# Performance work log

Measured on AMD Instinct MI355X. Metric: run time of the kernel, lower is better.

Reference implementation:

```python
import jax, jax.numpy as jnp
import numpy as np

N_NODES = 50000
N_EDGES = 800000
C = 96
L = 3


def setup_inputs() -> dict:
    key = jax.random.key(0)
    ks = jax.random.split(key, 7)
    x = jax.random.normal(ks[0], (N_NODES, C), dtype=jnp.float32)
    edge_index = jax.random.randint(ks[1], (2, N_EDGES), 0, N_NODES, dtype=jnp.int32)
    weight = jax.random.normal(ks[2], (L, C, C), dtype=jnp.float32) * (1.0 / np.sqrt(C))
    w_ih = jax.random.normal(ks[3], (3 * C, C), dtype=jnp.float32) * (1.0 / np.sqrt(C))
    w_hh = jax.random.normal(ks[4], (3 * C, C), dtype=jnp.float32) * (1.0 / np.sqrt(C))
    b_ih = jax.random.normal(ks[5], (3 * C,), dtype=jnp.float32) * 0.01
    b_hh = jax.random.normal(ks[6], (3 * C,), dtype=jnp.float32) * 0.01
    return {"x": x, "edge_index": edge_index, "weight": weight,
            "w_ih": w_ih, "w_hh": w_hh, "b_ih": b_ih, "b_hh": b_hh}


def _gru_cell(m, h, w_ih, w_hh, b_ih, b_hh):
    # PyTorch GRUCell math. gi/gh: [N, 3C]
    gi = m @ w_ih.T + b_ih
    gh = h @ w_hh.T + b_hh
    i_r, i_z, i_n = jnp.split(gi, 3, axis=-1)
    h_r, h_z, h_n = jnp.split(gh, 3, axis=-1)
    r = jax.nn.sigmoid(i_r + h_r)
    z = jax.nn.sigmoid(i_z + h_z)
    n = jnp.tanh(i_n + r * h_n)
    return (1.0 - z) * n + z * h


def reference(x, edge_index, weight, w_ih, w_hh, b_ih, b_hh):
    src = edge_index[0]  # message source (x_j)
    dst = edge_index[1]  # aggregation target
    for i in range(L):
        m = x @ weight[i]                                        # [N, C]
        agg = jax.ops.segment_sum(m[src], dst, num_segments=N_NODES)  # scatter-add
        x = _gru_cell(agg, x, w_ih, w_hh, b_ih, b_hh)
    return x
```

## Files before the change

kernel.cpp:

```cpp
#include <hip/hip_runtime.h>
#include <hip/hip_bf16.h>
#include <stdint.h>

#define NN 50000
#define NE 800000
#define CC 96
#define NL 3
#define NMT 3125

#define CAP 64
#define CAPSH 6

#define ELEMS_PER_LAYER 55296

#define FILL_GROUPS 8
#define FILL_GROUP_BLOCKS 400
#define FILL_BLOCKS (FILL_GROUPS*FILL_GROUP_BLOCKS)
#define NODES_PER_GROUP (NN/FILL_GROUPS)

#define PREP_ITEMS (NN*CC/8 + NL*288*CC + 288*CC)
#define PREP_BLOCKS ((PREP_ITEMS + 255)/256)

typedef _Float16 f16x8 __attribute__((ext_vector_type(8)));
typedef float f32x4 __attribute__((ext_vector_type(4)));
typedef uint16_t u16x8 __attribute__((ext_vector_type(8)));

__device__ __forceinline__ uint16_t f2h(float f){
  _Float16 h = (_Float16)f;
  return __builtin_bit_cast(uint16_t, h);
}
__device__ __forceinline__ float h2f(uint16_t u){
  return (float)__builtin_bit_cast(_Float16, u);
}

__device__ __forceinline__ size_t frag_elem(int tcol, int g2, int ks, int lane, int j){
  return (((size_t)(tcol*6 + g2)*3 + ks)*64 + lane)*8 + j;
}

__global__ void k_setup(const int* __restrict__ srcv, const int* __restrict__ dstv,
                        int* __restrict__ cursor, uint16_t* __restrict__ ssrc,
                        const float4* __restrict__ x, u16x8* __restrict__ xh,
                        const float* __restrict__ weight, const float* __restrict__ w_ih,
                        const float* __restrict__ w_hh, uint16_t* __restrict__ gw){
  if(blockIdx.x < FILL_BLOCKS){
    int g  = blockIdx.x & 7;
    int bg = blockIdx.x >> 3;
    int dlo = g * NODES_PER_GROUP;
    int dhi = dlo + NODES_PER_GROUP;
    const int tpg = FILL_GROUP_BLOCKS*256;
    for(int e = bg*256 + threadIdx.x; e < NE; e += tpg){
      int d = dstv[e];
      if(d >= dlo && d < dhi){
        int s = srcv[e];
        int pos = atomicAdd(&cursor[d], 1);
        if(pos < CAP) ssrc[((size_t)d << CAPSH) + pos] = (uint16_t)s;
      }
    }
    return;
  }
  int idx = (blockIdx.x - FILL_BLOCKS)*256 + threadIdx.x;
  const int N8 = NN*CC/8;
  if(idx < N8){
    float4 a = x[idx*2], b = x[idx*2+1];
    u16x8 o;
    o[0]=f2h(a.x); o[1]=f2h(a.y); o[2]=f2h(a.z); o[3]=f2h(a.w);
    o[4]=f2h(b.x); o[5]=f2h(b.y); o[6]=f2h(b.z); o[7]=f2h(b.w);
    xh[idx] = o;
    return;
  }
  int pidx = idx - N8;
  const int TOT1 = NL*288*CC;
  const int TOT2 = 288*CC;
  if(pidx < TOT1){
    int k = pidx % CC;
    int col = (pidx / CC) % 288;
    int l = pidx / (CC*288);
    const float4* wr = (const float4*)(weight + (size_t)(l*CC + k)*CC);
    const float4* ir = (const float4*)(w_ih + (size_t)col*CC);
    float acc = 0.f;
    #pragma unroll 4
    for(int k2=0;k2<CC/4;k2++){
      float4 a = wr[k2], b = ir[k2];
      acc += a.x*b.x + a.y*b.y + a.z*b.z + a.w*b.w;
    }
    int g = col / 96, cg = col % 96;
    int tcol = cg >> 4, n = cg & 15;
    int ks = k >> 5, r = (k & 31) >> 3, j = k & 7;
    int lane = r*16 + n;
    gw[(size_t)l*ELEMS_PER_LAYER + frag_elem(tcol, g, ks, lane, j)] = f2h(acc);
  } else {
    int idx2 = pidx - TOT1;
    if(idx2 < TOT2){
      int k = idx2 % CC;
      int col = idx2 / CC;
      uint16_t h = f2h(w_hh[(size_t)col*CC + k]);
      int g = col / 96, cg = col % 96;
      int tcol = cg >> 4, n = cg & 15;
      int ks = k >> 5, r = (k & 31) >> 3, j = k & 7;
      int lane = r*16 + n;
      size_t fe = frag_elem(tcol, 3+g, ks, lane, j);
      #pragma unroll
      for(int l=0;l<NL;l++) gw[(size_t)l*ELEMS_PER_LAYER + fe] = h;
    }
  }
}

#define MFMA16(A,B,C) __builtin_amdgcn_mfma_f32_16x16x32_f16(A,B,C,0,0,0)

__global__ __launch_bounds__(1024) void k_layer(
    const uint16_t* __restrict__ xh_cur, uint16_t* __restrict__ xh_nxt,
    const int* __restrict__ counts, const uint16_t* __restrict__ ssrc,
    const uint16_t* __restrict__ gw_l,
    const float* __restrict__ b_ih, const float* __restrict__ b_hh,
    float* __restrict__ out_f)
{
  __shared__ __align__(16) uint16_t lw[ELEMS_PER_LAYER];
  __shared__ u16x8 aggl[12*256];

  const int tid = threadIdx.x;
  const int wave = tid >> 6;
  const int lane = tid & 63;
  const int nidx = lane & 15;
  const int quad = lane >> 4;
  const int mtile = wave*256 + blockIdx.x;
  const bool valid = (mtile < NMT);
  const int mt = valid ? mtile : 0;

  f16x8 ax[3];
  {
    size_t arow = (size_t)(mt*16 + nidx)*CC;
    #pragma unroll
    for(int ks=0; ks<3; ks++)
      ax[ks] = *reinterpret_cast<const f16x8*>(xh_cur + arow + ks*32 + quad*8);
  }

  {
    const uint4* src = (const uint4*)gw_l;
    uint4* dst = (uint4*)lw;
    #pragma unroll
    for(int i=0;i<7;i++){
      int chunk = i*1024 + tid;
      if(chunk < ELEMS_PER_LAYER/8) dst[chunk] = src[chunk];
    }
  }

  {
    int nl_ = tid >> 2;
    int c8b = (tid & 3)*3;
    if(valid){
      int node = mt*16 + (nl_ & 15);
      int cnt = counts[node]; if(cnt > CAP) cnt = CAP;
      const u16x8* xg = (const u16x8*)xh_cur;
      float a0[8], a1[8], a2[8];
      #pragma unroll
      for(int t=0;t<8;t++){ a0[t]=0.f; a1[t]=0.f; a2[t]=0.f; }
      int j0 = node << CAPSH;
      int j1 = j0 + cnt;
      int j = j0;
      for(; j+4 <= j1; j+=4){
        ushort4 sv = *reinterpret_cast<const ushort4*>(ssrc + j);
        size_t b0 = (size_t)sv.x*12 + c8b;
        size_t b1 = (size_t)sv.y*12 + c8b;
        size_t b2 = (size_t)sv.z*12 + c8b;
        size_t b3 = (size_t)sv.w*12 + c8b;
        u16x8 v00=xg[b0], v01=xg[b0+1], v02=xg[b0+2];
        u16x8 v10=xg[b1], v11=xg[b1+1], v12=xg[b1+2];
        u16x8 v20=xg[b2], v21=xg[b2+1], v22=xg[b2+2];
        u16x8 v30=xg[b3], v31=xg[b3+1], v32=xg[b3+2];
        #pragma unroll
        for(int t=0;t<8;t++){
          a0[t] += (h2f(v00[t])+h2f(v10[t])) + (h2f(v20[t])+h2f(v30[t]));
          a1[t] += (h2f(v01[t])+h2f(v11[t])) + (h2f(v21[t])+h2f(v31[t]));
          a2[t] += (h2f(v02[t])+h2f(v12[t])) + (h2f(v22[t])+h2f(v32[t]));
        }
      }
      for(; j < j1; j++){
        size_t b = (size_t)ssrc[j]*12 + c8b;
        u16x8 v0=xg[b], v1=xg[b+1], v2=xg[b+2];
        #pragma unroll
        for(int t=0;t<8;t++){ a0[t]+=h2f(v0[t]); a1[t]+=h2f(v1[t]); a2[t]+=h2f(v2[t]); }
      }
      u16x8 w0, w1, w2;
      #pragma unroll
      for(int t=0;t<8;t++){ w0[t]=f2h(a0[t]); w1[t]=f2h(a1[t]); w2[t]=f2h(a2[t]); }
      aggl[(c8b+0)*256 + nl_] = w0;
      aggl[(c8b+1)*256 + nl_] = w1;
      aggl[(c8b+2)*256 + nl_] = w2;
    }
  }
  __syncthreads();
  if(!valid) return;

  f16x8 as[3];
  #pragma unroll
  for(int ks=0; ks<3; ks++)
    as[ks] = *reinterpret_cast<const f16x8*>(&aggl[(ks*4+quad)*256 + wave*16 + nidx]);

  #pragma unroll 1
  for(int tcol=0; tcol<6; tcol++){
    f32x4 air = {0.f,0.f,0.f,0.f}, aiz = {0.f,0.f,0.f,0.f}, ain = {0.f,0.f,0.f,0.f};
    f32x4 ahr = {0.f,0.f,0.f,0.f}, ahz = {0.f,0.f,0.f,0.f}, ahn = {0.f,0.f,0.f,0.f};

    #pragma unroll
    for(int ks=0; ks<3; ks++){
      const uint16_t* base = lw + (((size_t)tcol*6)*3 + ks)*512 + lane*8;
      #define BFRAG(g2) (*reinterpret_cast<const f16x8*>(base + (size_t)(g2)*3*512))
      air = MFMA16(as[ks], BFRAG(0), air);
      aiz = MFMA16(as[ks], BFRAG(1), aiz);
      ain = MFMA16(as[ks], BFRAG(2), ain);
      ahr = MFMA16(ax[ks], BFRAG(3), ahr);
      ahz = MFMA16(ax[ks], BFRAG(4), ahz);
      ahn = MFMA16(ax[ks], BFRAG(5), ahn);
      #undef BFRAG
    }

    int c = tcol*16 + nidx;
    float bir_ = b_ih[c], biz_ = b_ih[CC+c], bin_ = b_ih[2*CC+c];
    float bhr_ = b_hh[c], bhz_ = b_hh[CC+c], bhn_ = b_hh[2*CC+c];

    #pragma unroll
    for(int r=0;r<4;r++){
      int node = mtile*16 + quad*4 + r;
      float ir  = air[r] + bir_;
      float iz  = aiz[r] + biz_;
      float in_ = ain[r] + bin_;
      float hr  = ahr[r] + bhr_;
      float hz  = ahz[r] + bhz_;
      float hn  = ahn[r] + bhn_;
      float rg = 1.f/(1.f + __expf(-(ir+hr)));
      float zg = 1.f/(1.f + __expf(-(iz+hz)));
      float nv = in_ + rg*hn;
      float av = fminf(fabsf(nv), 15.f);
      float e2 = __expf(2.f*av);
      float tg = 1.f - 2.f/(e2 + 1.f);
      tg = (nv < 0.f)? -tg : tg;
      size_t oi = (size_t)node*CC + c;
      float hp = h2f(xh_cur[oi]);
      float h = (1.f - zg)*tg + zg*hp;
      if(out_f) out_f[oi] = h;
      else      xh_nxt[oi] = f2h(h);
    }
  }
}

extern "C" void kernel_launch(void* const* d_in, const int* in_sizes, int n_in,
                              void* d_out, int out_size, void* d_ws, size_t ws_size,
                              hipStream_t stream){
  const float* x0     = (const float*)d_in[0];
  const int*   ei     = (const int*)d_in[1];
  const float* weight = (const float*)d_in[2];
  const float* w_ih   = (const float*)d_in[3];
  const float* w_hh   = (const float*)d_in[4];
  const float* b_ih   = (const float*)d_in[5];
  const float* b_hh   = (const float*)d_in[6];
  float* out = (float*)d_out;

  const int* srcv = ei;
  const int* dstv = ei + NE;

  char* ws = (char*)d_ws;
  size_t off = 0;
  auto carve = [&](size_t bytes)->char*{
    char* p = ws + off;
    off += (bytes + 255) & ~(size_t)255;
    return p;
  };
  int* cursor     = (int*)carve((size_t)NN*4);
  uint16_t* ssrc  = (uint16_t*)carve((size_t)NN*CAP*2);
  uint16_t* xh16A = (uint16_t*)carve((size_t)NN*CC*2);
  uint16_t* xh16B = (uint16_t*)carve((size_t)NN*CC*2);
  uint16_t* gw    = (uint16_t*)carve((size_t)NL*ELEMS_PER_LAYER*2);

  hipMemsetAsync(cursor, 0, (size_t)NN*4, stream);
  k_setup<<<FILL_BLOCKS + PREP_BLOCKS, 256, 0, stream>>>(
      srcv, dstv, cursor, ssrc, (const float4*)x0, (u16x8*)xh16A, weight, w_ih, w_hh, gw);

  uint16_t* xh_cur = xh16A;
  uint16_t* xh_nxt = xh16B;
  for(int l=0; l<NL; l++){
    float* out_f = (l==NL-1) ? out : nullptr;
    k_layer<<<256, 1024, 0, stream>>>(xh_cur, xh_nxt, cursor, ssrc,
                                      gw + (size_t)l*ELEMS_PER_LAYER,
                                      b_ih, b_hh, out_f);
    uint16_t* t = xh_cur; xh_cur = xh_nxt; xh_nxt = t;
  }
}
```

Baseline: 256.6 us.

## Fuse setup and all layers into one cooperative persistent kernel with grid syncs

Replaces the separate setup kernel and the three per-layer launches with a single cooperative kernel of 256x1024 threads that uses grid.sync between phases. The CSR fill and the fp16 conversion/weight prep now run as grid-stride loops inside it. The aggregation is remapped so each lane gathers directly into its MFMA A-fragment layout, which removes the LDS staging buffer for the aggregate. The intent is to cut launch gaps and the LDS round trip. The cost is grid-wide barriers, reliance on cooperative launch residency, and far fewer threads doing the atomic edge-fill phase.

```diff
diff --git a/kernel.cpp b/kernel.cpp
--- a/kernel.cpp
+++ b/kernel.cpp
@@ -1,6 +1,8 @@
 #include <hip/hip_runtime.h>
-#include <hip/hip_bf16.h>
+#include <hip/hip_cooperative_groups.h>
 #include <stdint.h>
+
+namespace cg = cooperative_groups;
 
 #define NN 50000
 #define NE 800000
@@ -13,13 +15,10 @@
 
 #define ELEMS_PER_LAYER 55296
 
-#define FILL_GROUPS 8
-#define FILL_GROUP_BLOCKS 400
-#define FILL_BLOCKS (FILL_GROUPS*FILL_GROUP_BLOCKS)
-#define NODES_PER_GROUP (NN/FILL_GROUPS)
-
+#define NODES_PER_GROUP (NN/8)
+#define GRID_BLOCKS 256
+#define BLOCK_THREADS 1024
 #define PREP_ITEMS (NN*CC/8 + NL*288*CC + 288*CC)
-#define PREP_BLOCKS ((PREP_ITEMS + 255)/256)
 
 typedef _Float16 f16x8 __attribute__((ext_vector_type(8)));
 typedef float f32x4 __attribute__((ext_vector_type(4)));
@@ -37,136 +36,141 @@
   return (((size_t)(tcol*6 + g2)*3 + ks)*64 + lane)*8 + j;
 }
 
-__global__ void k_setup(const int* __restrict__ srcv, const int* __restrict__ dstv,
-                        int* __restrict__ cursor, uint16_t* __restrict__ ssrc,
-                        const float4* __restrict__ x, u16x8* __restrict__ xh,
-                        const float* __restrict__ weight, const float* __restrict__ w_ih,
-                        const float* __restrict__ w_hh, uint16_t* __restrict__ gw){
-  if(blockIdx.x < FILL_BLOCKS){
-    int g  = blockIdx.x & 7;
-    int bg = blockIdx.x >> 3;
-    int dlo = g * NODES_PER_GROUP;
-    int dhi = dlo + NODES_PER_GROUP;
-    const int tpg = FILL_GROUP_BLOCKS*256;
-    for(int e = bg*256 + threadIdx.x; e < NE; e += tpg){
-      int d = dstv[e];
-      if(d >= dlo && d < dhi){
-        int s = srcv[e];
-        int pos = atomicAdd(&cursor[d], 1);
-        if(pos < CAP) ssrc[((size_t)d << CAPSH) + pos] = (uint16_t)s;
-      }
-    }
-    return;
-  }
-  int idx = (blockIdx.x - FILL_BLOCKS)*256 + threadIdx.x;
-  const int N8 = NN*CC/8;
-  if(idx < N8){
-    float4 a = x[idx*2], b = x[idx*2+1];
-    u16x8 o;
-    o[0]=f2h(a.x); o[1]=f2h(a.y); o[2]=f2h(a.z); o[3]=f2h(a.w);
-    o[4]=f2h(b.x); o[5]=f2h(b.y); o[6]=f2h(b.z); o[7]=f2h(b.w);
-    xh[idx] = o;
-    return;
-  }
-  int pidx = idx - N8;
-  const int TOT1 = NL*288*CC;
-  const int TOT2 = 288*CC;
-  if(pidx < TOT1){
-    int k = pidx % CC;
-    int col = (pidx / CC) % 288;
-    int l = pidx / (CC*288);
-    const float4* wr = (const float4*)(weight + (size_t)(l*CC + k)*CC);
-    const float4* ir = (const float4*)(w_ih + (size_t)col*CC);
-    float acc = 0.f;
-    #pragma unroll 4
-    for(int k2=0;k2<CC/4;k2++){
-      float4 a = wr[k2], b = ir[k2];
-      acc += a.x*b.x + a.y*b.y + a.z*b.z + a.w*b.w;
-    }
-    int g = col / 96, cg = col % 96;
-    int tcol = cg >> 4, n = cg & 15;
-    int ks = k >> 5, r = (k & 31) >> 3, j = k & 7;
-    int lane = r*16 + n;
-    gw[(size_t)l*ELEMS_PER_LAYER + frag_elem(tcol, g, ks, lane, j)] = f2h(acc);
-  } else {
-    int idx2 = pidx - TOT1;
-    if(idx2 < TOT2){
-      int k = idx2 % CC;
-      int col = idx2 / CC;
-      uint16_t h = f2h(w_hh[(size_t)col*CC + k]);
-      int g = col / 96, cg = col % 96;
-      int tcol = cg >> 4, n = cg & 15;
-      int ks = k >> 5, r = (k & 31) >> 3, j = k & 7;
-      int lane = r*16 + n;
-      size_t fe = frag_elem(tcol, 3+g, ks, lane, j);
-      #pragma unroll
-      for(int l=0;l<NL;l++) gw[(size_t)l*ELEMS_PER_LAYER + fe] = h;
-    }
-  }
-}
-
 #define MFMA16(A,B,C) __builtin_amdgcn_mfma_f32_16x16x32_f16(A,B,C,0,0,0)
 
-__global__ __launch_bounds__(1024) void k_layer(
-    const uint16_t* __restrict__ xh_cur, uint16_t* __restrict__ xh_nxt,
-    const int* __restrict__ counts, const uint16_t* __restrict__ ssrc,
-    const uint16_t* __restrict__ gw_l,
+__global__ __launch_bounds__(1024) void k_fused(
+    const int* __restrict__ srcv, const int* __restrict__ dstv,
+    int* __restrict__ cursor, uint16_t* __restrict__ ssrc,
+    const float4* __restrict__ x4,
+    const float* __restrict__ weight, const float* __restrict__ w_ih,
+    const float* __restrict__ w_hh, uint16_t* __restrict__ gw,
+    uint16_t* __restrict__ xhA, uint16_t* __restrict__ xhB,
     const float* __restrict__ b_ih, const float* __restrict__ b_hh,
-    float* __restrict__ out_f)
+    float* __restrict__ out)
 {
+  cg::grid_group grid = cg::this_grid();
   __shared__ __align__(16) uint16_t lw[ELEMS_PER_LAYER];
-  __shared__ u16x8 aggl[12*256];
-
-  const int tid = threadIdx.x;
+
+  const int tid  = threadIdx.x;
+  const int bid  = blockIdx.x;
   const int wave = tid >> 6;
   const int lane = tid & 63;
   const int nidx = lane & 15;
   const int quad = lane >> 4;
-  const int mtile = wave*256 + blockIdx.x;
+
+  {
+    int g  = bid & 7;
+    int bg = bid >> 3;
+    int dlo = g * NODES_PER_GROUP;
+    #pragma unroll 4
+    for(int e = bg*BLOCK_THREADS + tid; e < NE; e += 32*BLOCK_THREADS){
+      int d = dstv[e];
+      if((unsigned)(d - dlo) < (unsigned)NODES_PER_GROUP){
+        int s = srcv[e];
+        int pos = atomicAdd(&cursor[d], 1);
+        if(pos < CAP) ssrc[((size_t)d << CAPSH) + pos] = (uint16_t)s;
+      }
+    }
+  }
+  {
+    u16x8* xh = (u16x8*)xhA;
+    const int N8   = NN*CC/8;
+    const int TOT1 = NL*288*CC;
+    const int TOT2 = 288*CC;
+    for(int idx = bid*BLOCK_THREADS + tid; idx < PREP_ITEMS;
+        idx += GRID_BLOCKS*BLOCK_THREADS){
+      if(idx < N8){
+        float4 a = x4[idx*2], b = x4[idx*2+1];
+        u16x8 o;
+        o[0]=f2h(a.x); o[1]=f2h(a.y); o[2]=f2h(a.z); o[3]=f2h(a.w);
+        o[4]=f2h(b.x); o[5]=f2h(b.y); o[6]=f2h(b.z); o[7]=f2h(b.w);
+        xh[idx] = o;
+      } else {
+        int pidx = idx - N8;
+        if(pidx < TOT1){
+          int k = pidx % CC;
+          int col = (pidx / CC) % 288;
+          int l = pidx / (CC*288);
+          const float4* wr = (const float4*)(weight + (size_t)(l*CC + k)*CC);
+          const float4* ir = (const float4*)(w_ih + (size_t)col*CC);
+          float acc = 0.f;
+          #pragma unroll 4
+          for(int k2=0;k2<CC/4;k2++){
+            float4 a = wr[k2], b = ir[k2];
+            acc += a.x*b.x + a.y*b.y + a.z*b.z + a.w*b.w;
+          }
+          int g = col / 96, cg = col % 96;
+          int tcol = cg >> 4, n = cg & 15;
+          int ks = k >> 5, r = (k & 31) >> 3, j = k & 7;
+          int ln = r*16 + n;
+          gw[(size_t)l*ELEMS_PER_LAYER + frag_elem(tcol, g, ks, ln, j)] = f2h(acc);
+        } else {
+          int idx2 = pidx - TOT1;
+          if(idx2 < TOT2){
+            int k = idx2 % CC;
+            int col = idx2 / CC;
+            uint16_t h = f2h(w_hh[(size_t)col*CC + k]);
+            int g = col / 96, cg = col % 96;
+            int tcol = cg >> 4, n = cg & 15;
+            int ks = k >> 5, r = (k & 31) >> 3, j = k & 7;
+            int ln = r*16 + n;
+            size_t fe = frag_elem(tcol, 3+g, ks, ln, j);
+            #pragma unroll
+            for(int l=0;l<NL;l++) gw[(size_t)l*ELEMS_PER_LAYER + fe] = h;
+          }
+        }
+      }
+    }
+  }
+  grid.sync();
+
+  const int mtile = wave*256 + bid;
   const bool valid = (mtile < NMT);
   const int mt = valid ? mtile : 0;
-
-  f16x8 ax[3];
-  {
-    size_t arow = (size_t)(mt*16 + nidx)*CC;
+  uint16_t* cur = xhA;
+  uint16_t* nxt = xhB;
+
+  for(int l=0; l<NL; l++){
+    const uint16_t* gw_l = gw + (size_t)l*ELEMS_PER_LAYER;
+
+    f16x8 ax[3];
+    {
+      size_t arow = (size_t)(mt*16 + nidx)*CC;
+      #pragma unroll
+      for(int ks=0; ks<3; ks++)
+        ax[ks] = *reinterpret_cast<const f16x8*>(cur + arow + ks*32 + quad*8);
+    }
+
+    {
+      const uint4* src = (const uint4*)gw_l;
+      uint4* dst = (uint4*)lw;
+      #pragma unroll
+      for(int i=0;i<7;i++){
+        int chunk = i*1024 + tid;
+        if(chunk < ELEMS_PER_LAYER/8) dst[chunk] = src[chunk];
+      }
+    }
+
+    float a0[8], a1[8], a2[8];
     #pragma unroll
-    for(int ks=0; ks<3; ks++)
-      ax[ks] = *reinterpret_cast<const f16x8*>(xh_cur + arow + ks*32 + quad*8);
-  }
-
-  {
-    const uint4* src = (const uint4*)gw_l;
-    uint4* dst = (uint4*)lw;
-    #pragma unroll
-    for(int i=0;i<7;i++){
-      int chunk = i*1024 + tid;
-      if(chunk < ELEMS_PER_LAYER/8) dst[chunk] = src[chunk];
-    }
-  }
-
-  {
-    int nl_ = tid >> 2;
-    int c8b = (tid & 3)*3;
+    for(int t=0;t<8;t++){ a0[t]=0.f; a1[t]=0.f; a2[t]=0.f; }
     if(valid){
-      int node = mt*16 + (nl_ & 15);
-      int cnt = counts[node]; if(cnt > CAP) cnt = CAP;
-      const u16x8* xg = (const u16x8*)xh_cur;
-      float a0[8], a1[8], a2[8];
-      #pragma unroll
-      for(int t=0;t<8;t++){ a0[t]=0.f; a1[t]=0.f; a2[t]=0.f; }
+      int node = mt*16 + nidx;
+      int cnt = cursor[node]; if(cnt > CAP) cnt = CAP;
+      const u16x8* xg = (const u16x8*)cur;
       int j0 = node << CAPSH;
       int j1 = j0 + cnt;
       int j = j0;
       for(; j+4 <= j1; j+=4){
         ushort4 sv = *reinterpret_cast<const ushort4*>(ssrc + j);
-        size_t b0 = (size_t)sv.x*12 + c8b;
-        size_t b1 = (size_t)sv.y*12 + c8b;
-        size_t b2 = (size_t)sv.z*12 + c8b;
-        size_t b3 = (size_t)sv.w*12 + c8b;
-        u16x8 v00=xg[b0], v01=xg[b0+1], v02=xg[b0+2];
-        u16x8 v10=xg[b1], v11=xg[b1+1], v12=xg[b1+2];
-        u16x8 v20=xg[b2], v21=xg[b2+1], v22=xg[b2+2];
-        u16x8 v30=xg[b3], v31=xg[b3+1], v32=xg[b3+2];
+        size_t b0 = (size_t)sv.x*12 + quad;
+        size_t b1 = (size_t)sv.y*12 + quad;
+        size_t b2 = (size_t)sv.z*12 + quad;
+        size_t b3 = (size_t)sv.w*12 + quad;
+        u16x8 v00=xg[b0],   v01=xg[b0+4], v02=xg[b0+8];
+        u16x8 v10=xg[b1],   v11=xg[b1+4], v12=xg[b1+8];
+        u16x8 v20=xg[b2],   v21=xg[b2+4], v22=xg[b2+8];
+        u16x8 v30=xg[b3],   v31=xg[b3+4], v32=xg[b3+8];
         #pragma unroll
         for(int t=0;t<8;t++){
           a0[t] += (h2f(v00[t])+h2f(v10[t])) + (h2f(v20[t])+h2f(v30[t]));
@@ -175,71 +179,70 @@
         }
       }
       for(; j < j1; j++){
-        size_t b = (size_t)ssrc[j]*12 + c8b;
-        u16x8 v0=xg[b], v1=xg[b+1], v2=xg[b+2];
+        size_t b = (size_t)ssrc[j]*12 + quad;
+        u16x8 v0=xg[b], v1=xg[b+4], v2=xg[b+8];
         #pragma unroll
         for(int t=0;t<8;t++){ a0[t]+=h2f(v0[t]); a1[t]+=h2f(v1[t]); a2[t]+=h2f(v2[t]); }
       }
-      u16x8 w0, w1, w2;
+    }
+    __syncthreads();
+
+    if(valid){
+      f16x8 as[3];
       #pragma unroll
-      for(int t=0;t<8;t++){ w0[t]=f2h(a0[t]); w1[t]=f2h(a1[t]); w2[t]=f2h(a2[t]); }
-      aggl[(c8b+0)*256 + nl_] = w0;
-      aggl[(c8b+1)*256 + nl_] = w1;
-      aggl[(c8b+2)*256 + nl_] = w2;
-    }
-  }
-  __syncthreads();
-  if(!valid) return;
-
-  f16x8 as[3];
-  #pragma unroll
-  for(int ks=0; ks<3; ks++)
-    as[ks] = *reinterpret_cast<const f16x8*>(&aggl[(ks*4+quad)*256 + wave*16 + nidx]);
-
-  #pragma unroll 1
-  for(int tcol=0; tcol<6; tcol++){
-    f32x4 air = {0.f,0.f,0.f,0.f}, aiz = {0.f,0.f,0.f,0.f}, ain = {0.f,0.f,0.f,0.f};
-    f32x4 ahr = {0.f,0.f,0.f,0.f}, ahz = {0.f,0.f,0.f,0.f}, ahn = {0.f,0.f,0.f,0.f};
-
-    #pragma unroll
-    for(int ks=0; ks<3; ks++){
-      const uint16_t* base = lw + (((size_t)tcol*6)*3 + ks)*512 + lane*8;
-      #define BFRAG(g2) (*reinterpret_cast<const f16x8*>(base + (size_t)(g2)*3*512))
-      air = MFMA16(as[ks], BFRAG(0), air);
-      aiz = MFMA16(as[ks], BFRAG(1), aiz);
-      ain = MFMA16(as[ks], BFRAG(2), ain);
-      ahr = MFMA16(ax[ks], BFRAG(3), ahr);
-      ahz = MFMA16(ax[ks], BFRAG(4), ahz);
-      ahn = MFMA16(ax[ks], BFRAG(5), ahn);
-      #undef BFRAG
-    }
-
-    int c = tcol*16 + nidx;
-    float bir_ = b_ih[c], biz_ = b_ih[CC+c], bin_ = b_ih[2*CC+c];
-    float bhr_ = b_hh[c], bhz_ = b_hh[CC+c], bhn_ = b_hh[2*CC+c];
-
-    #pragma unroll
-    for(int r=0;r<4;r++){
-      int node = mtile*16 + quad*4 + r;
-      float ir  = air[r] + bir_;
-      float iz  = aiz[r] + biz_;
-      float in_ = ain[r] + bin_;
-      float hr  = ahr[r] + bhr_;
-      float hz  = ahz[r] + bhz_;
-      float hn  = ahn[r] + bhn_;
-      float rg = 1.f/(1.f + __expf(-(ir+hr)));
-      float zg = 1.f/(1.f + __expf(-(iz+hz)));
-      float nv = in_ + rg*hn;
-      float av = fminf(fabsf(nv), 15.f);
-      float e2 = __expf(2.f*av);
-      float tg = 1.f - 2.f/(e2 + 1.f);
-      tg = (nv < 0.f)? -tg : tg;
-      size_t oi = (size_t)node*CC + c;
-      float hp = h2f(xh_cur[oi]);
-      float h = (1.f - zg)*tg + zg*hp;
-      if(out_f) out_f[oi] = h;
-      else      xh_nxt[oi] = f2h(h);
-    }
+      for(int t=0;t<8;t++){
+        as[0][t]=(_Float16)a0[t]; as[1][t]=(_Float16)a1[t]; as[2][t]=(_Float16)a2[t];
+      }
+
+      #pragma unroll 1
+      for(int tcol=0; tcol<6; tcol++){
+        f32x4 air = {0.f,0.f,0.f,0.f}, aiz = {0.f,0.f,0.f,0.f}, ain = {0.f,0.f,0.f,0.f};
+        f32x4 ahr = {0.f,0.f,0.f,0.f}, ahz = {0.f,0.f,0.f,0.f}, ahn = {0.f,0.f,0.f,0.f};
+
+        #pragma unroll
+        for(int ks=0; ks<3; ks++){
+          const uint16_t* base = lw + (((size_t)tcol*6)*3 + ks)*512 + lane*8;
+          #define BFRAG(g2) (*reinterpret_cast<const f16x8*>(base + (size_t)(g2)*3*512))
+          air = MFMA16(as[ks], BFRAG(0), air);
+          aiz = MFMA16(as[ks], BFRAG(1), aiz);
+          ain = MFMA16(as[ks], BFRAG(2), ain);
+          ahr = MFMA16(ax[ks], BFRAG(3), ahr);
+          ahz = MFMA16(ax[ks], BFRAG(4), ahz);
+          ahn = MFMA16(ax[ks], BFRAG(5), ahn);
+          #undef BFRAG
+        }
+
+        int c = tcol*16 + nidx;
+        float bir_ = b_ih[c], biz_ = b_ih[CC+c], bin_ = b_ih[2*CC+c];
+        float bhr_ = b_hh[c], bhz_ = b_hh[CC+c], bhn_ = b_hh[2*CC+c];
+
+        #pragma unroll
+        for(int r=0;r<4;r++){
+          int node = mtile*16 + quad*4 + r;
+          float ir  = air[r] + bir_;
+          float iz  = aiz[r] + biz_;
+          float in_ = ain[r] + bin_;
+          float hr  = ahr[r] + bhr_;
+          float hz  = ahz[r] + bhz_;
+          float hn  = ahn[r] + bhn_;
+          float rg = 1.f/(1.f + __expf(-(ir+hr)));
+          float zg = 1.f/(1.f + __expf(-(iz+hz)));
+          float nv = in_ + rg*hn;
+          float av = fminf(fabsf(nv), 15.f);
+          float e2 = __expf(2.f*av);
+          float tg = 1.f - 2.f/(e2 + 1.f);
+          tg = (nv < 0.f)? -tg : tg;
+          size_t oi = (size_t)node*CC + c;
+          float hp = h2f(cur[oi]);
+          float h = (1.f - zg)*tg + zg*hp;
+          if(l == NL-1) out[oi] = h;
+          else          nxt[oi] = f2h(h);
+        }
+      }
+    }
+
+    if(l < NL-1) grid.sync();
+    uint16_t* tswap = cur; cur = nxt; nxt = tswap;
   }
 }
 
@@ -267,21 +270,19 @@
   };
   int* cursor     = (int*)carve((size_t)NN*4);
   uint16_t* ssrc  = (uint16_t*)carve((size_t)NN*CAP*2);
-  uint16_t* xh16A = (uint16_t*)carve((size_t)NN*CC*2);
-  uint16_t* xh16B = (uint16_t*)carve((size_t)NN*CC*2);
+  uint16_t* xhA   = (uint16_t*)carve((size_t)NN*CC*2);
+  uint16_t* xhB   = (uint16_t*)carve((size_t)NN*CC*2);
   uint16_t* gw    = (uint16_t*)carve((size_t)NL*ELEMS_PER_LAYER*2);
 
   hipMemsetAsync(cursor, 0, (size_t)NN*4, stream);
-  k_setup<<<FILL_BLOCKS + PREP_BLOCKS, 256, 0, stream>>>(
-      srcv, dstv, cursor, ssrc, (const float4*)x0, (u16x8*)xh16A, weight, w_ih, w_hh, gw);
-
-  uint16_t* xh_cur = xh16A;
-  uint16_t* xh_nxt = xh16B;
-  for(int l=0; l<NL; l++){
-    float* out_f = (l==NL-1) ? out : nullptr;
-    k_layer<<<256, 1024, 0, stream>>>(xh_cur, xh_nxt, cursor, ssrc,
-                                      gw + (size_t)l*ELEMS_PER_LAYER,
-                                      b_ih, b_hh, out_f);
-    uint16_t* t = xh_cur; xh_cur = xh_nxt; xh_nxt = t;
-  }
-}
+
+  const float4* x4 = (const float4*)x0;
+  void* args[] = {
+    (void*)&srcv, (void*)&dstv, (void*)&cursor, (void*)&ssrc,
+    (void*)&x4, (void*)&weight, (void*)&w_ih, (void*)&w_hh, (void*)&gw,
+    (void*)&xhA, (void*)&xhB, (void*)&b_ih, (void*)&b_hh, (void*)&out
+  };
+  hipLaunchCooperativeKernel((const void*)k_fused,
+                             dim3(GRID_BLOCKS), dim3(BLOCK_THREADS),
+                             args, 0, stream);
+}
```

After: 364.9 us. +42.2%, slower.

## Bucket edges with shared-memory counters per node range, drop cursor memset

Applied to the files above, without the earlier changes.

The CSR-like fill now uses 64 blocks, each owning a 784-node range. Each block scans all destinations with int4 loads and increments per-node counters in LDS instead of doing global atomics, then writes the final counts to the cursor array. This removes the separate memset launch and the global atomic traffic. The cost is that every fill block reads the full 800K-entry destination array, and only 64 blocks do the fill, which may leave the GPU underused and make the fill phase the critical path. Prep blocks are also resized to 1024 threads.

```diff
diff --git a/kernel.cpp b/kernel.cpp
--- a/kernel.cpp
+++ b/kernel.cpp
@@ -13,13 +13,10 @@
 
 #define ELEMS_PER_LAYER 55296
 
-#define FILL_GROUPS 8
-#define FILL_GROUP_BLOCKS 400
-#define FILL_BLOCKS (FILL_GROUPS*FILL_GROUP_BLOCKS)
-#define NODES_PER_GROUP (NN/FILL_GROUPS)
-
+#define FILL_BLOCKS 64
+#define NPG 784
 #define PREP_ITEMS (NN*CC/8 + NL*288*CC + 288*CC)
-#define PREP_BLOCKS ((PREP_ITEMS + 255)/256)
+#define PREP_BLOCKS ((PREP_ITEMS + 1023)/1024)
 
 typedef _Float16 f16x8 __attribute__((ext_vector_type(8)));
 typedef float f32x4 __attribute__((ext_vector_type(4)));
@@ -37,28 +34,40 @@
   return (((size_t)(tcol*6 + g2)*3 + ks)*64 + lane)*8 + j;
 }
 
-__global__ void k_setup(const int* __restrict__ srcv, const int* __restrict__ dstv,
-                        int* __restrict__ cursor, uint16_t* __restrict__ ssrc,
-                        const float4* __restrict__ x, u16x8* __restrict__ xh,
-                        const float* __restrict__ weight, const float* __restrict__ w_ih,
-                        const float* __restrict__ w_hh, uint16_t* __restrict__ gw){
+__global__ __launch_bounds__(1024) void k_setup(
+    const int* __restrict__ srcv, const int* __restrict__ dstv,
+    int* __restrict__ cursor, uint16_t* __restrict__ ssrc,
+    const float4* __restrict__ x, u16x8* __restrict__ xh,
+    const float* __restrict__ weight, const float* __restrict__ w_ih,
+    const float* __restrict__ w_hh, uint16_t* __restrict__ gw){
+  __shared__ int lcnt[NPG];
+  const int tid = threadIdx.x;
   if(blockIdx.x < FILL_BLOCKS){
-    int g  = blockIdx.x & 7;
-    int bg = blockIdx.x >> 3;
-    int dlo = g * NODES_PER_GROUP;
-    int dhi = dlo + NODES_PER_GROUP;
-    const int tpg = FILL_GROUP_BLOCKS*256;
-    for(int e = bg*256 + threadIdx.x; e < NE; e += tpg){
-      int d = dstv[e];
-      if(d >= dlo && d < dhi){
-        int s = srcv[e];
-        int pos = atomicAdd(&cursor[d], 1);
-        if(pos < CAP) ssrc[((size_t)d << CAPSH) + pos] = (uint16_t)s;
-      }
+    int g = blockIdx.x;
+    int dlo = g * NPG;
+    for(int i = tid; i < NPG; i += 1024) lcnt[i] = 0;
+    __syncthreads();
+    const int4* d4 = (const int4*)dstv;
+    for(int i = tid; i < NE/4; i += 1024){
+      int4 d = d4[i];
+      int e = 4*i;
+      unsigned r0 = (unsigned)(d.x - dlo);
+      unsigned r1 = (unsigned)(d.y - dlo);
+      unsigned r2 = (unsigned)(d.z - dlo);
+      unsigned r3 = (unsigned)(d.w - dlo);
+      if(r0 < NPG){ int p = atomicAdd(&lcnt[r0],1); if(p < CAP) ssrc[((size_t)(dlo+(int)r0) << CAPSH) + p] = (uint16_t)srcv[e+0]; }
+      if(r1 < NPG){ int p = atomicAdd(&lcnt[r1],1); if(p < CAP) ssrc[((size_t)(dlo+(int)r1) << CAPSH) + p] = (uint16_t)srcv[e+1]; }
+      if(r2 < NPG){ int p = atomicAdd(&lcnt[r2],1); if(p < CAP) ssrc[((size_t)(dlo+(int)r2) << CAPSH) + p] = (uint16_t)srcv[e+2]; }
+      if(r3 < NPG){ int p = atomicAdd(&lcnt[r3],1); if(p < CAP) ssrc[((size_t)(dlo+(int)r3) << CAPSH) + p] = (uint16_t)srcv[e+3]; }
+    }
+    __syncthreads();
+    for(int i = tid; i < NPG; i += 1024){
+      int node = dlo + i;
+      if(node < NN) cursor[node] = lcnt[i];
     }
     return;
   }
-  int idx = (blockIdx.x - FILL_BLOCKS)*256 + threadIdx.x;
+  int idx = (blockIdx.x - FILL_BLOCKS)*1024 + tid;
   const int N8 = NN*CC/8;
   if(idx < N8){
     float4 a = x[idx*2], b = x[idx*2+1];
@@ -271,8 +280,7 @@
   uint16_t* xh16B = (uint16_t*)carve((size_t)NN*CC*2);
   uint16_t* gw    = (uint16_t*)carve((size_t)NL*ELEMS_PER_LAYER*2);
 
-  hipMemsetAsync(cursor, 0, (size_t)NN*4, stream);
-  k_setup<<<FILL_BLOCKS + PREP_BLOCKS, 256, 0, stream>>>(
+  k_setup<<<FILL_BLOCKS + PREP_BLOCKS, 1024, 0, stream>>>(
       srcv, dstv, cursor, ssrc, (const float4*)x0, (u16x8*)xh16A, weight, w_ih, w_hh, gw);
 
   uint16_t* xh_cur = xh16A;
```

Result: slower. 422.4 us (+64.6%).

## Gather neighbours directly into MFMA fragments and read GRU weights from global

Applied to the files above, without the earlier changes.

The layer kernel no longer stages the ~110KB per-layer weight fragments into LDS or passes aggregated features through shared memory. Each lane now gathers the neighbour features for exactly the channels its MFMA A-fragment needs and converts them to fp16 in registers, and B fragments are loaded straight from global memory (relying on L2/L1 caching). Blocks shrink to 256 threads with one m-tile per wave, so there are more, smaller blocks and no __syncthreads. This removes the large per-block LDS copy and the block barrier, and the small LDS footprint should allow more concurrent blocks. In exchange, every wave re-reads the weight fragments from cache, and the gather access pattern per lane changes.

```diff
diff --git a/kernel.cpp b/kernel.cpp
--- a/kernel.cpp
+++ b/kernel.cpp
@@ -107,94 +107,69 @@
 
 #define MFMA16(A,B,C) __builtin_amdgcn_mfma_f32_16x16x32_f16(A,B,C,0,0,0)
 
-__global__ __launch_bounds__(1024) void k_layer(
+__global__ __launch_bounds__(256) void k_layer(
     const uint16_t* __restrict__ xh_cur, uint16_t* __restrict__ xh_nxt,
     const int* __restrict__ counts, const uint16_t* __restrict__ ssrc,
     const uint16_t* __restrict__ gw_l,
     const float* __restrict__ b_ih, const float* __restrict__ b_hh,
     float* __restrict__ out_f)
 {
-  __shared__ __align__(16) uint16_t lw[ELEMS_PER_LAYER];
-  __shared__ u16x8 aggl[12*256];
-
-  const int tid = threadIdx.x;
+  const int tid  = threadIdx.x;
   const int wave = tid >> 6;
   const int lane = tid & 63;
   const int nidx = lane & 15;
   const int quad = lane >> 4;
-  const int mtile = wave*256 + blockIdx.x;
-  const bool valid = (mtile < NMT);
-  const int mt = valid ? mtile : 0;
+  const int mtile = blockIdx.x*4 + wave;
+  if(mtile >= NMT) return;
+
+  float a0[8], a1[8], a2[8];
+  #pragma unroll
+  for(int t=0;t<8;t++){ a0[t]=0.f; a1[t]=0.f; a2[t]=0.f; }
+  {
+    int node = mtile*16 + nidx;
+    int cnt = counts[node]; if(cnt > CAP) cnt = CAP;
+    const u16x8* xg = (const u16x8*)xh_cur;
+    int j0 = node << CAPSH;
+    int j1 = j0 + cnt;
+    int j = j0;
+    for(; j+4 <= j1; j+=4){
+      ushort4 sv = *reinterpret_cast<const ushort4*>(ssrc + j);
+      size_t b0 = (size_t)sv.x*12 + quad;
+      size_t b1 = (size_t)sv.y*12 + quad;
+      size_t b2 = (size_t)sv.z*12 + quad;
+      size_t b3 = (size_t)sv.w*12 + quad;
+      u16x8 v00=xg[b0],   v01=xg[b0+4], v02=xg[b0+8];
+      u16x8 v10=xg[b1],   v11=xg[b1+4], v12=xg[b1+8];
+      u16x8 v20=xg[b2],   v21=xg[b2+4], v22=xg[b2+8];
+      u16x8 v30=xg[b3],   v31=xg[b3+4], v32=xg[b3+8];
+      #pragma unroll
+      for(int t=0;t<8;t++){
+        a0[t] += (h2f(v00[t])+h2f(v10[t])) + (h2f(v20[t])+h2f(v30[t]));
+        a1[t] += (h2f(v01[t])+h2f(v11[t])) + (h2f(v21[t])+h2f(v31[t]));
+        a2[t] += (h2f(v02[t])+h2f(v12[t])) + (h2f(v22[t])+h2f(v32[t]));
+      }
+    }
+    for(; j < j1; j++){
+      size_t b = (size_t)ssrc[j]*12 + quad;
+      u16x8 v0=xg[b], v1=xg[b+4], v2=xg[b+8];
+      #pragma unroll
+      for(int t=0;t<8;t++){ a0[t]+=h2f(v0[t]); a1[t]+=h2f(v1[t]); a2[t]+=h2f(v2[t]); }
+    }
+  }
 
   f16x8 ax[3];
   {
-    size_t arow = (size_t)(mt*16 + nidx)*CC;
+    size_t arow = (size_t)(mtile*16 + nidx)*CC;
     #pragma unroll
     for(int ks=0; ks<3; ks++)
       ax[ks] = *reinterpret_cast<const f16x8*>(xh_cur + arow + ks*32 + quad*8);
   }
 
-  {
-    const uint4* src = (const uint4*)gw_l;
-    uint4* dst = (uint4*)lw;
-    #pragma unroll
-    for(int i=0;i<7;i++){
-      int chunk = i*1024 + tid;
-      if(chunk < ELEMS_PER_LAYER/8) dst[chunk] = src[chunk];
-    }
-  }
-
-  {
-    int nl_ = tid >> 2;
-    int c8b = (tid & 3)*3;
-    if(valid){
-      int node = mt*16 + (nl_ & 15);
-      int cnt = counts[node]; if(cnt > CAP) cnt = CAP;
-      const u16x8* xg = (const u16x8*)xh_cur;
-      float a0[8], a1[8], a2[8];
-      #pragma unroll
-      for(int t=0;t<8;t++){ a0[t]=0.f; a1[t]=0.f; a2[t]=0.f; }
-      int j0 = node << CAPSH;
-      int j1 = j0 + cnt;
-      int j = j0;
-      for(; j+4 <= j1; j+=4){
-        ushort4 sv = *reinterpret_cast<const ushort4*>(ssrc + j);
-        size_t b0 = (size_t)sv.x*12 + c8b;
-        size_t b1 = (size_t)sv.y*12 + c8b;
-        size_t b2 = (size_t)sv.z*12 + c8b;
-        size_t b3 = (size_t)sv.w*12 + c8b;
-        u16x8 v00=xg[b0], v01=xg[b0+1], v02=xg[b0+2];
-        u16x8 v10=xg[b1], v11=xg[b1+1], v12=xg[b1+2];
-        u16x8 v20=xg[b2], v21=xg[b2+1], v22=xg[b2+2];
-        u16x8 v30=xg[b3], v31=xg[b3+1], v32=xg[b3+2];
-        #pragma unroll
-        for(int t=0;t<8;t++){
-          a0[t] += (h2f(v00[t])+h2f(v10[t])) + (h2f(v20[t])+h2f(v30[t]));
-          a1[t] += (h2f(v01[t])+h2f(v11[t])) + (h2f(v21[t])+h2f(v31[t]));
-          a2[t] += (h2f(v02[t])+h2f(v12[t])) + (h2f(v22[t])+h2f(v32[t]));
-        }
-      }
-      for(; j < j1; j++){
-        size_t b = (size_t)ssrc[j]*12 + c8b;
-        u16x8 v0=xg[b], v1=xg[b+1], v2=xg[b+2];
-        #pragma unroll
-        for(int t=0;t<8;t++){ a0[t]+=h2f(v0[t]); a1[t]+=h2f(v1[t]); a2[t]+=h2f(v2[t]); }
-      }
-      u16x8 w0, w1, w2;
-      #pragma unroll
-      for(int t=0;t<8;t++){ w0[t]=f2h(a0[t]); w1[t]=f2h(a1[t]); w2[t]=f2h(a2[t]); }
-      aggl[(c8b+0)*256 + nl_] = w0;
-      aggl[(c8b+1)*256 + nl_] = w1;
-      aggl[(c8b+2)*256 + nl_] = w2;
-    }
-  }
-  __syncthreads();
-  if(!valid) return;
-
   f16x8 as[3];
   #pragma unroll
-  for(int ks=0; ks<3; ks++)
-    as[ks] = *reinterpret_cast<const f16x8*>(&aggl[(ks*4+quad)*256 + wave*16 + nidx]);
+  for(int t=0;t<8;t++){
+    as[0][t]=(_Float16)a0[t]; as[1][t]=(_Float16)a1[t]; as[2][t]=(_Float16)a2[t];
+  }
 
   #pragma unroll 1
   for(int tcol=0; tcol<6; tcol++){
@@ -203,7 +178,7 @@
 
     #pragma unroll
     for(int ks=0; ks<3; ks++){
-      const uint16_t* base = lw + (((size_t)tcol*6)*3 + ks)*512 + lane*8;
+      const uint16_t* base = gw_l + (((size_t)tcol*6)*3 + ks)*512 + lane*8;
       #define BFRAG(g2) (*reinterpret_cast<const f16x8*>(base + (size_t)(g2)*3*512))
       air = MFMA16(as[ks], BFRAG(0), air);
       aiz = MFMA16(as[ks], BFRAG(1), aiz);
@@ -277,11 +252,12 @@
 
   uint16_t* xh_cur = xh16A;
   uint16_t* xh_nxt = xh16B;
+  const int LAYER_BLOCKS = (NMT + 3)/4;
   for(int l=0; l<NL; l++){
     float* out_f = (l==NL-1) ? out : nullptr;
-    k_layer<<<256, 1024, 0, stream>>>(xh_cur, xh_nxt, cursor, ssrc,
-                                      gw + (size_t)l*ELEMS_PER_LAYER,
-                                      b_ih, b_hh, out_f);
+    k_layer<<<LAYER_BLOCKS, 256, 0, stream>>>(xh_cur, xh_nxt, cursor, ssrc,
+                                              gw + (size_t)l*ELEMS_PER_LAYER,
+                                              b_ih, b_hh, out_f);
     uint16_t* t = xh_cur; xh_cur = xh_nxt; xh_nxt = t;
   }
 }
```

Result: slower. 270.6 us (+5.4%).
